# Kernel optimization log

Hardware: AMD Instinct MI355X
Metric: run time of the kernel (lower is better)

The kernel has to match this reference:

```python
import jax, jax.numpy as jnp
import numpy as np

B, T, E, H = 8, 2048, 1024, 64

def setup_inputs() -> dict:
    key = jax.random.key(0)
    k1, k2, k3, k4 = jax.random.split(key, 4)
    x = jax.random.normal(k1, (B, T, E), dtype=jnp.float32)
    # Linear(E, H, bias=False) weights stored as [E, H] (x @ W)
    s = 1.0 / np.sqrt(E)
    Wk = jax.random.normal(k2, (E, H), dtype=jnp.float32) * s
    Wq = jax.random.normal(k3, (E, H), dtype=jnp.float32) * s
    Wv = jax.random.normal(k4, (E, H), dtype=jnp.float32) * s
    return {"x": x, "Wk": Wk, "Wq": Wq, "Wv": Wv}

def reference(x, Wk, Wq, Wv):
    _, t, e = x.shape
    k = jnp.einsum('bte,eh->bth', x, Wk)
    q = jnp.einsum('bte,eh->bth', x, Wq)
    v = jnp.einsum('bte,eh->bth', x, Wv)
    # NOTE: original scales by E**-0.5 (embedding dim), not head_size**-0.5
    wei = jnp.einsum('bqh,bkh->bqk', q, k) * (e ** -0.5)
    causal = jnp.tril(jnp.ones((t, t), dtype=bool))
    wei = jnp.where(causal, wei, -jnp.inf)
    wei = jax.nn.softmax(wei, axis=-1)
    out = jnp.einsum('bqk,bkh->bqh', wei, v)
    return out
```

## Files before the change

kernel.cpp:

```cpp
#include <hip/hip_runtime.h>

typedef unsigned short u16;
typedef unsigned int u32;
typedef __bf16 bf16x8 __attribute__((ext_vector_type(8)));
typedef __bf16 bf16x4 __attribute__((ext_vector_type(4)));
typedef float f32x4 __attribute__((ext_vector_type(4)));

constexpr int Bn = 8, Tn = 2048, En = 1024, Hn = 64;
constexpr int Mrows = Bn * Tn;
constexpr float CEXP = 0.03125f * 1.4426950408889634f;

__device__ __forceinline__ u16 f2bf(float f) {
  u32 u = __float_as_uint(f);
  return (u16)((u + 0x7fffu + ((u >> 16) & 1u)) >> 16);
}

__device__ __forceinline__ void gload16(const void* g, void* l) {
  __builtin_amdgcn_global_load_lds(
      (const __attribute__((address_space(1))) void*)g,
      (__attribute__((address_space(3))) void*)l, 16, 0, 0);
}

__global__ __launch_bounds__(256) void wt_kernel(
    const float* __restrict__ Wk, const float* __restrict__ Wq,
    const float* __restrict__ Wv, u16* __restrict__ Wt) {
  __shared__ u16 tile[64][72];
  const int mat = blockIdx.x >> 4;
  const int k0 = (blockIdx.x & 15) * 64;
  const float* W = (mat == 0) ? Wk : (mat == 1) ? Wq : Wv;
  const int t = threadIdx.x;
  {
    const int kl = t >> 2;
    const int h0 = (t & 3) * 16;
    const float4* src = (const float4*)(W + (size_t)(k0 + kl) * Hn + h0);
#pragma unroll
    for (int i = 0; i < 4; ++i) {
      float4 v = src[i];
      tile[h0 + 4 * i + 0][kl] = f2bf(v.x);
      tile[h0 + 4 * i + 1][kl] = f2bf(v.y);
      tile[h0 + 4 * i + 2][kl] = f2bf(v.z);
      tile[h0 + 4 * i + 3][kl] = f2bf(v.w);
    }
  }
  __syncthreads();
  {
    const int hl = t >> 2;
    const int kk = (t & 3) * 16;
    uint4 a = *(const uint4*)&tile[hl][kk];
    uint4 b = *(const uint4*)&tile[hl][kk + 8];
    u16* dst = Wt + (size_t)mat * Hn * En + (size_t)hl * En + k0 + kk;
    *(uint4*)dst = a;
    *(uint4*)(dst + 8) = b;
  }
}

__global__ __launch_bounds__(256, 2) void qkv_kernel(
    const float* __restrict__ x, const u16* __restrict__ Wt,
    u16* __restrict__ Kb16, u16* __restrict__ Qb16, u16* __restrict__ Vt16) {
  constexpr int BK = 64;
  __shared__ __align__(16) float xs[3][32 * BK];
  const int t = threadIdx.x;
  const int w = t >> 6, lane = t & 63;
  const int quad = lane >> 4, l16 = lane & 15;
  const int r0 = blockIdx.x * 32;

  const int rj0 = w * 8 + (lane >> 4);
  const int rj1 = rj0 + 4;
  const float* gsrc0 = x + (size_t)(r0 + rj0) * En + (((lane & 15) ^ (rj0 & 15)) << 2);
  const float* gsrc1 = x + (size_t)(r0 + rj1) * En + (((lane & 15) ^ (rj1 & 15)) << 2);

  const u16* wpb = Wt + (size_t)l16 * En + quad * 8;

  int ofs[2][2];
#pragma unroll
  for (int ks = 0; ks < 2; ++ks) {
    ofs[ks][0] = ((ks * 8 + quad * 2) ^ l16) << 2;
    ofs[ks][1] = ((ks * 8 + quad * 2 + 1) ^ l16) << 2;
  }

  f32x4 acc[3][2];
#pragma unroll
  for (int i = 0; i < 3; ++i)
#pragma unroll
    for (int nt = 0; nt < 2; ++nt) acc[i][nt] = (f32x4){0.f, 0.f, 0.f, 0.f};

  bf16x8 afA[3][2], afB[3][2];

#define STAGE(P, K0)                              \
  do {                                            \
    gload16(gsrc0 + (K0), (P) + w * 512);         \
    gload16(gsrc1 + (K0), (P) + w * 512 + 256);   \
  } while (0)

#define LOADA(DST, K0)                                                              \
  do {                                                                              \
    _Pragma("unroll") for (int i_ = 0; i_ < 3; ++i_)                                \
        _Pragma("unroll") for (int ks_ = 0; ks_ < 2; ++ks_)                         \
            DST[i_][ks_] = *(const bf16x8*)(wpb + (size_t)((3 * w + i_) * 16) * En + \
                                            (K0) + ks_ * 32);                       \
  } while (0)

#define CVT8(LO, HI, R)                                       \
  do {                                                        \
    R[0] = (__bf16)LO[0]; R[1] = (__bf16)LO[1];               \
    R[2] = (__bf16)LO[2]; R[3] = (__bf16)LO[3];               \
    R[4] = (__bf16)HI[0]; R[5] = (__bf16)HI[1];               \
    R[6] = (__bf16)HI[2]; R[7] = (__bf16)HI[3];               \
  } while (0)

#define COMPUTE(P, AF)                                                             \
  do {                                                                             \
    const float* xa_ = (P) + l16 * 64;                                             \
    const float* xb_ = (P) + (l16 + 16) * 64;                                      \
    _Pragma("unroll") for (int ks_ = 0; ks_ < 2; ++ks_) {                          \
      f32x4 lo0_ = *(const f32x4*)(xa_ + ofs[ks_][0]);                             \
      f32x4 hi0_ = *(const f32x4*)(xa_ + ofs[ks_][1]);                             \
      f32x4 lo1_ = *(const f32x4*)(xb_ + ofs[ks_][0]);                             \
      f32x4 hi1_ = *(const f32x4*)(xb_ + ofs[ks_][1]);                             \
      bf16x8 b0_, b1_;                                                             \
      CVT8(lo0_, hi0_, b0_);                                                       \
      CVT8(lo1_, hi1_, b1_);                                                       \
      _Pragma("unroll") for (int i_ = 0; i_ < 3; ++i_) {                           \
        acc[i_][0] = __builtin_amdgcn_mfma_f32_16x16x32_bf16(AF[i_][ks_], b0_,     \
                                                             acc[i_][0], 0, 0, 0); \
        acc[i_][1] = __builtin_amdgcn_mfma_f32_16x16x32_bf16(AF[i_][ks_], b1_,     \
                                                             acc[i_][1], 0, 0, 0); \
      }                                                                            \
    }                                                                              \
  } while (0)

#define WAITBAR(N)                                          \
  do {                                                      \
    asm volatile("s_waitcnt vmcnt(" #N ")" ::: "memory");   \
    __builtin_amdgcn_s_barrier();                           \
    asm volatile("" ::: "memory");                          \
  } while (0)

  float* p0 = &xs[0][0];
  float* p1 = &xs[1][0];
  float* p2 = &xs[2][0];

  STAGE(p0, 0);
  STAGE(p1, BK);
  LOADA(afA, 0);

  for (int tt = 0; tt < 16; tt += 2) {
    WAITBAR(8);
    LOADA(afB, (tt + 1) * 64);
    asm volatile("" ::: "memory");
    if (tt + 2 < 16) STAGE(p2, (tt + 2) * 64);
    COMPUTE(p0, afA);

    if (tt == 14) {
      WAITBAR(6);
    } else {
      WAITBAR(8);
    }
    if (tt + 2 < 16) LOADA(afA, (tt + 2) * 64);
    asm volatile("" ::: "memory");
    if (tt + 3 < 16) STAGE(p0, (tt + 3) * 64);
    COMPUTE(p1, afB);

    float* tmp = p0; p0 = p2; p2 = p1; p1 = tmp;
  }

#undef STAGE
#undef LOADA
#undef CVT8
#undef COMPUTE
#undef WAITBAR

#pragma unroll
  for (int i = 0; i < 3; ++i) {
    const int mt = 3 * w + i;
    const int mat = mt >> 2, ht = mt & 3;
#pragma unroll
    for (int nt = 0; nt < 2; ++nt) {
      const int row = r0 + nt * 16 + l16;
      f32x4 a = acc[i][nt];
      if (mat < 2) {
        u16* dst = ((mat == 0) ? Kb16 : Qb16) + (size_t)row * Hn + ht * 16 + quad * 4;
        uint2 pk;
        pk.x = (u32)f2bf(a[0]) | ((u32)f2bf(a[1]) << 16);
        pk.y = (u32)f2bf(a[2]) | ((u32)f2bf(a[3]) << 16);
        *(uint2*)dst = pk;
      } else {
        const int bb = row >> 11, tt = row & 2047;
        u16* base = Vt16 + ((size_t)bb * 64) * Tn + tt;
#pragma unroll
        for (int r = 0; r < 4; ++r)
          base[(size_t)(ht * 16 + quad * 4 + r) * Tn] = f2bf(a[r]);
      }
    }
  }
}

__global__ __launch_bounds__(256, 4) void attn_kernel(
    const u16* __restrict__ Qb16, const u16* __restrict__ Kb16,
    const u16* __restrict__ Vt16, float* __restrict__ out) {
  __shared__ u16 pt[2][4][16][40];
  __shared__ float l_sh[4][16];
  __shared__ float o_sh[4][16][68];

  const int idx = blockIdx.x;
  const int b = idx & 7;
  const int tq = 127 - (idx >> 3);
  const int w = threadIdx.x >> 6, lane = threadIdx.x & 63;
  const int quad = lane >> 4, l16 = lane & 15;
  const int qbase = tq * 16;
  const int limit = qbase + 16;
  const int ch = ((limit + 127) >> 7) << 5;
  const int lo = w * ch;
  const int hi = min(lo + ch, limit);
  const int q_abs = qbase + l16;

  const u16* Kp = Kb16 + (size_t)b * Tn * Hn;
  const u16* Vp = Vt16 + (size_t)b * 64 * Tn;

  const u16* qrow = Qb16 + ((size_t)b * Tn + q_abs) * Hn + quad * 8;
  const bf16x8 qb0 = *(const bf16x8*)(qrow);
  const bf16x8 qb1 = *(const bf16x8*)(qrow + 32);

  f32x4 od0 = {0.f, 0.f, 0.f, 0.f}, od1 = od0, od2 = od0, od3 = od0;
  f32x4 lacc = {0.f, 0.f, 0.f, 0.f};

#pragma unroll 2
  for (int kb = lo; kb < hi; kb += 32) {
    const int par = (kb >> 5) & 1;
    const u16* krow0 = Kp + (size_t)(kb + l16) * Hn + quad * 8;
    const u16* krow1 = krow0 + (size_t)16 * Hn;
    f32x4 z = {0.f, 0.f, 0.f, 0.f};
    f32x4 st0 = __builtin_amdgcn_mfma_f32_16x16x32_bf16(*(const bf16x8*)(krow0), qb0, z, 0, 0, 0);
    st0 = __builtin_amdgcn_mfma_f32_16x16x32_bf16(*(const bf16x8*)(krow0 + 32), qb1, st0, 0, 0, 0);
    f32x4 st1 = __builtin_amdgcn_mfma_f32_16x16x32_bf16(*(const bf16x8*)(krow1), qb0, z, 0, 0, 0);
    st1 = __builtin_amdgcn_mfma_f32_16x16x32_bf16(*(const bf16x8*)(krow1 + 32), qb1, st1, 0, 0, 0);

    if (kb + 15 > qbase) {
#pragma unroll
      for (int r = 0; r < 4; ++r)
        if (kb + quad * 4 + r > q_abs) st0[r] = -3.0e38f;
    }
    if (kb + 31 > qbase) {
#pragma unroll
      for (int r = 0; r < 4; ++r)
        if (kb + 16 + quad * 4 + r > q_abs) st1[r] = -3.0e38f;
    }

    f32x4 p0, p1;
#pragma unroll
    for (int r = 0; r < 4; ++r) {
      p0[r] = __builtin_amdgcn_exp2f(st0[r] * CEXP);
      p1[r] = __builtin_amdgcn_exp2f(st1[r] * CEXP);
    }
    lacc += p0;
    lacc += p1;

    {
      bf16x4 w0, w1;
      w0[0] = (__bf16)p0[0]; w0[1] = (__bf16)p0[1];
      w0[2] = (__bf16)p0[2]; w0[3] = (__bf16)p0[3];
      w1[0] = (__bf16)p1[0]; w1[1] = (__bf16)p1[1];
      w1[2] = (__bf16)p1[2]; w1[3] = (__bf16)p1[3];
      *(bf16x4*)&pt[par][w][l16][quad * 4] = w0;
      *(bf16x4*)&pt[par][w][l16][16 + quad * 4] = w1;
    }
    const bf16x8 pb = *(const bf16x8*)&pt[par][w][l16][quad * 8];

    const u16* vrow = Vp + (size_t)l16 * Tn + kb + quad * 8;
    od0 = __builtin_amdgcn_mfma_f32_16x16x32_bf16(*(const bf16x8*)(vrow), pb, od0, 0, 0, 0);
    od1 = __builtin_amdgcn_mfma_f32_16x16x32_bf16(*(const bf16x8*)(vrow + (size_t)16 * Tn), pb, od1, 0, 0, 0);
    od2 = __builtin_amdgcn_mfma_f32_16x16x32_bf16(*(const bf16x8*)(vrow + (size_t)32 * Tn), pb, od2, 0, 0, 0);
    od3 = __builtin_amdgcn_mfma_f32_16x16x32_bf16(*(const bf16x8*)(vrow + (size_t)48 * Tn), pb, od3, 0, 0, 0);
  }

  float l = (lacc[0] + lacc[1]) + (lacc[2] + lacc[3]);
  l += __shfl_xor(l, 16);
  l += __shfl_xor(l, 32);
  if (quad == 0) l_sh[w][l16] = l;
  *(f32x4*)&o_sh[w][l16][0 * 16 + quad * 4] = od0;
  *(f32x4*)&o_sh[w][l16][1 * 16 + quad * 4] = od1;
  *(f32x4*)&o_sh[w][l16][2 * 16 + quad * 4] = od2;
  *(f32x4*)&o_sh[w][l16][3 * 16 + quad * 4] = od3;
  __syncthreads();

  const int qq = threadIdx.x >> 4, dq = threadIdx.x & 15;
  float lg = 0.f;
  f32x4 acc = {0.f, 0.f, 0.f, 0.f};
#pragma unroll
  for (int ww = 0; ww < 4; ++ww) {
    lg += l_sh[ww][qq];
    acc += *(const f32x4*)&o_sh[ww][qq][dq * 4];
  }
  acc *= (1.f / lg);
  *(f32x4*)(out + ((size_t)b * Tn + qbase + qq) * Hn + dq * 4) = acc;
}

extern "C" void kernel_launch(void* const* d_in, const int* in_sizes, int n_in,
                              void* d_out, int out_size, void* d_ws, size_t ws_size,
                              hipStream_t stream) {
  const void* x = nullptr;
  const void* Ws[3] = {nullptr, nullptr, nullptr};
  int wj = 0;
  for (int i = 0; i < n_in; ++i) {
    if (in_sizes[i] == Bn * Tn * En) x = d_in[i];
    else if (wj < 3) Ws[wj++] = d_in[i];
  }
  const float* Wk = (const float*)Ws[0];
  const float* Wq = (const float*)Ws[1];
  const float* Wv = (const float*)Ws[2];

  u16* Kb16 = (u16*)d_ws;
  u16* Qb16 = Kb16 + (size_t)Mrows * Hn;
  u16* Vt16 = Qb16 + (size_t)Mrows * Hn;
  u16* Wt   = Vt16 + (size_t)Mrows * Hn;

  wt_kernel<<<48, 256, 0, stream>>>(Wk, Wq, Wv, Wt);
  qkv_kernel<<<Mrows / 32, 256, 0, stream>>>((const float*)x, Wt, Kb16, Qb16, Vt16);
  attn_kernel<<<Bn * (Tn / 16), 256, 0, stream>>>(Qb16, Kb16, Vt16, (float*)d_out);
}
```

Before: 155.2 us.

## Process two 16-row query tiles per attention block to reuse K/V loads

Each attention block now handles 32 query rows (two 16-row tiles) instead of 16, so every K and V fragment loaded from global memory feeds MFMAs for both tiles. This halves the grid size and roughly halves K/V global traffic per query. In exchange, register pressure rises (eight output accumulators) and occupancy drops (launch bounds lowered from 4 to 2 blocks per CU). The second tile also computes some fully masked keys at the diagonal.

```diff
diff --git a/kernel.cpp b/kernel.cpp
--- a/kernel.cpp
+++ b/kernel.cpp
@@ -195,104 +195,161 @@
   }
 }
 
-__global__ __launch_bounds__(256, 4) void attn_kernel(
+__global__ __launch_bounds__(256, 2) void attn_kernel(
     const u16* __restrict__ Qb16, const u16* __restrict__ Kb16,
     const u16* __restrict__ Vt16, float* __restrict__ out) {
-  __shared__ u16 pt[2][4][16][40];
-  __shared__ float l_sh[4][16];
-  __shared__ float o_sh[4][16][68];
+  __shared__ u16 pt[2][4][2][16][40];
+  __shared__ float l_sh[2][4][16];
+  __shared__ float o_sh[2][4][16][68];
 
   const int idx = blockIdx.x;
   const int b = idx & 7;
-  const int tq = 127 - (idx >> 3);
+  const int tq = 63 - (idx >> 3);
   const int w = threadIdx.x >> 6, lane = threadIdx.x & 63;
   const int quad = lane >> 4, l16 = lane & 15;
-  const int qbase = tq * 16;
-  const int limit = qbase + 16;
+  const int qbase = tq * 32;
+  const int limit = qbase + 32;
   const int ch = ((limit + 127) >> 7) << 5;
   const int lo = w * ch;
   const int hi = min(lo + ch, limit);
-  const int q_abs = qbase + l16;
+  const int qa_abs = qbase + l16;
+  const int qb_abs = qbase + 16 + l16;
 
   const u16* Kp = Kb16 + (size_t)b * Tn * Hn;
   const u16* Vp = Vt16 + (size_t)b * 64 * Tn;
 
-  const u16* qrow = Qb16 + ((size_t)b * Tn + q_abs) * Hn + quad * 8;
-  const bf16x8 qb0 = *(const bf16x8*)(qrow);
-  const bf16x8 qb1 = *(const bf16x8*)(qrow + 32);
-
-  f32x4 od0 = {0.f, 0.f, 0.f, 0.f}, od1 = od0, od2 = od0, od3 = od0;
-  f32x4 lacc = {0.f, 0.f, 0.f, 0.f};
+  const u16* qrowA = Qb16 + ((size_t)b * Tn + qa_abs) * Hn + quad * 8;
+  const u16* qrowB = qrowA + (size_t)16 * Hn;
+  const bf16x8 qa0 = *(const bf16x8*)(qrowA);
+  const bf16x8 qa1 = *(const bf16x8*)(qrowA + 32);
+  const bf16x8 qb0 = *(const bf16x8*)(qrowB);
+  const bf16x8 qb1 = *(const bf16x8*)(qrowB + 32);
+
+  f32x4 oA0 = {0.f, 0.f, 0.f, 0.f}, oA1 = oA0, oA2 = oA0, oA3 = oA0;
+  f32x4 oB0 = oA0, oB1 = oA0, oB2 = oA0, oB3 = oA0;
+  f32x4 laccA = oA0, laccB = oA0;
 
 #pragma unroll 2
   for (int kb = lo; kb < hi; kb += 32) {
     const int par = (kb >> 5) & 1;
     const u16* krow0 = Kp + (size_t)(kb + l16) * Hn + quad * 8;
     const u16* krow1 = krow0 + (size_t)16 * Hn;
-    f32x4 z = {0.f, 0.f, 0.f, 0.f};
-    f32x4 st0 = __builtin_amdgcn_mfma_f32_16x16x32_bf16(*(const bf16x8*)(krow0), qb0, z, 0, 0, 0);
-    st0 = __builtin_amdgcn_mfma_f32_16x16x32_bf16(*(const bf16x8*)(krow0 + 32), qb1, st0, 0, 0, 0);
-    f32x4 st1 = __builtin_amdgcn_mfma_f32_16x16x32_bf16(*(const bf16x8*)(krow1), qb0, z, 0, 0, 0);
-    st1 = __builtin_amdgcn_mfma_f32_16x16x32_bf16(*(const bf16x8*)(krow1 + 32), qb1, st1, 0, 0, 0);
+    const bf16x8 k0lo = *(const bf16x8*)(krow0);
+    const bf16x8 k0hi = *(const bf16x8*)(krow0 + 32);
+    const bf16x8 k1lo = *(const bf16x8*)(krow1);
+    const bf16x8 k1hi = *(const bf16x8*)(krow1 + 32);
+
+    const f32x4 z = {0.f, 0.f, 0.f, 0.f};
+    f32x4 s0a = __builtin_amdgcn_mfma_f32_16x16x32_bf16(k0lo, qa0, z, 0, 0, 0);
+    s0a = __builtin_amdgcn_mfma_f32_16x16x32_bf16(k0hi, qa1, s0a, 0, 0, 0);
+    f32x4 s1a = __builtin_amdgcn_mfma_f32_16x16x32_bf16(k1lo, qa0, z, 0, 0, 0);
+    s1a = __builtin_amdgcn_mfma_f32_16x16x32_bf16(k1hi, qa1, s1a, 0, 0, 0);
+    f32x4 s0b = __builtin_amdgcn_mfma_f32_16x16x32_bf16(k0lo, qb0, z, 0, 0, 0);
+    s0b = __builtin_amdgcn_mfma_f32_16x16x32_bf16(k0hi, qb1, s0b, 0, 0, 0);
+    f32x4 s1b = __builtin_amdgcn_mfma_f32_16x16x32_bf16(k1lo, qb0, z, 0, 0, 0);
+    s1b = __builtin_amdgcn_mfma_f32_16x16x32_bf16(k1hi, qb1, s1b, 0, 0, 0);
 
     if (kb + 15 > qbase) {
 #pragma unroll
       for (int r = 0; r < 4; ++r)
-        if (kb + quad * 4 + r > q_abs) st0[r] = -3.0e38f;
+        if (kb + quad * 4 + r > qa_abs) s0a[r] = -3.0e38f;
     }
     if (kb + 31 > qbase) {
 #pragma unroll
       for (int r = 0; r < 4; ++r)
-        if (kb + 16 + quad * 4 + r > q_abs) st1[r] = -3.0e38f;
-    }
-
-    f32x4 p0, p1;
+        if (kb + 16 + quad * 4 + r > qa_abs) s1a[r] = -3.0e38f;
+    }
+    if (kb + 15 > qbase + 16) {
+#pragma unroll
+      for (int r = 0; r < 4; ++r)
+        if (kb + quad * 4 + r > qb_abs) s0b[r] = -3.0e38f;
+    }
+    if (kb + 31 > qbase + 16) {
+#pragma unroll
+      for (int r = 0; r < 4; ++r)
+        if (kb + 16 + quad * 4 + r > qb_abs) s1b[r] = -3.0e38f;
+    }
+
+    f32x4 pa0, pa1, pb0v, pb1v;
 #pragma unroll
     for (int r = 0; r < 4; ++r) {
-      p0[r] = __builtin_amdgcn_exp2f(st0[r] * CEXP);
-      p1[r] = __builtin_amdgcn_exp2f(st1[r] * CEXP);
-    }
-    lacc += p0;
-    lacc += p1;
+      pa0[r] = __builtin_amdgcn_exp2f(s0a[r] * CEXP);
+      pa1[r] = __builtin_amdgcn_exp2f(s1a[r] * CEXP);
+      pb0v[r] = __builtin_amdgcn_exp2f(s0b[r] * CEXP);
+      pb1v[r] = __builtin_amdgcn_exp2f(s1b[r] * CEXP);
+    }
+    laccA += pa0;
+    laccA += pa1;
+    laccB += pb0v;
+    laccB += pb1v;
 
     {
-      bf16x4 w0, w1;
-      w0[0] = (__bf16)p0[0]; w0[1] = (__bf16)p0[1];
-      w0[2] = (__bf16)p0[2]; w0[3] = (__bf16)p0[3];
-      w1[0] = (__bf16)p1[0]; w1[1] = (__bf16)p1[1];
-      w1[2] = (__bf16)p1[2]; w1[3] = (__bf16)p1[3];
-      *(bf16x4*)&pt[par][w][l16][quad * 4] = w0;
-      *(bf16x4*)&pt[par][w][l16][16 + quad * 4] = w1;
-    }
-    const bf16x8 pb = *(const bf16x8*)&pt[par][w][l16][quad * 8];
+      bf16x4 wa0, wa1, wb0, wb1;
+      wa0[0] = (__bf16)pa0[0]; wa0[1] = (__bf16)pa0[1];
+      wa0[2] = (__bf16)pa0[2]; wa0[3] = (__bf16)pa0[3];
+      wa1[0] = (__bf16)pa1[0]; wa1[1] = (__bf16)pa1[1];
+      wa1[2] = (__bf16)pa1[2]; wa1[3] = (__bf16)pa1[3];
+      wb0[0] = (__bf16)pb0v[0]; wb0[1] = (__bf16)pb0v[1];
+      wb0[2] = (__bf16)pb0v[2]; wb0[3] = (__bf16)pb0v[3];
+      wb1[0] = (__bf16)pb1v[0]; wb1[1] = (__bf16)pb1v[1];
+      wb1[2] = (__bf16)pb1v[2]; wb1[3] = (__bf16)pb1v[3];
+      *(bf16x4*)&pt[par][w][0][l16][quad * 4] = wa0;
+      *(bf16x4*)&pt[par][w][0][l16][16 + quad * 4] = wa1;
+      *(bf16x4*)&pt[par][w][1][l16][quad * 4] = wb0;
+      *(bf16x4*)&pt[par][w][1][l16][16 + quad * 4] = wb1;
+    }
+    const bf16x8 pba = *(const bf16x8*)&pt[par][w][0][l16][quad * 8];
+    const bf16x8 pbb = *(const bf16x8*)&pt[par][w][1][l16][quad * 8];
 
     const u16* vrow = Vp + (size_t)l16 * Tn + kb + quad * 8;
-    od0 = __builtin_amdgcn_mfma_f32_16x16x32_bf16(*(const bf16x8*)(vrow), pb, od0, 0, 0, 0);
-    od1 = __builtin_amdgcn_mfma_f32_16x16x32_bf16(*(const bf16x8*)(vrow + (size_t)16 * Tn), pb, od1, 0, 0, 0);
-    od2 = __builtin_amdgcn_mfma_f32_16x16x32_bf16(*(const bf16x8*)(vrow + (size_t)32 * Tn), pb, od2, 0, 0, 0);
-    od3 = __builtin_amdgcn_mfma_f32_16x16x32_bf16(*(const bf16x8*)(vrow + (size_t)48 * Tn), pb, od3, 0, 0, 0);
-  }
-
-  float l = (lacc[0] + lacc[1]) + (lacc[2] + lacc[3]);
-  l += __shfl_xor(l, 16);
-  l += __shfl_xor(l, 32);
-  if (quad == 0) l_sh[w][l16] = l;
-  *(f32x4*)&o_sh[w][l16][0 * 16 + quad * 4] = od0;
-  *(f32x4*)&o_sh[w][l16][1 * 16 + quad * 4] = od1;
-  *(f32x4*)&o_sh[w][l16][2 * 16 + quad * 4] = od2;
-  *(f32x4*)&o_sh[w][l16][3 * 16 + quad * 4] = od3;
+    const bf16x8 v0 = *(const bf16x8*)(vrow);
+    const bf16x8 v1 = *(const bf16x8*)(vrow + (size_t)16 * Tn);
+    const bf16x8 v2 = *(const bf16x8*)(vrow + (size_t)32 * Tn);
+    const bf16x8 v3 = *(const bf16x8*)(vrow + (size_t)48 * Tn);
+
+    oA0 = __builtin_amdgcn_mfma_f32_16x16x32_bf16(v0, pba, oA0, 0, 0, 0);
+    oA1 = __builtin_amdgcn_mfma_f32_16x16x32_bf16(v1, pba, oA1, 0, 0, 0);
+    oA2 = __builtin_amdgcn_mfma_f32_16x16x32_bf16(v2, pba, oA2, 0, 0, 0);
+    oA3 = __builtin_amdgcn_mfma_f32_16x16x32_bf16(v3, pba, oA3, 0, 0, 0);
+    oB0 = __builtin_amdgcn_mfma_f32_16x16x32_bf16(v0, pbb, oB0, 0, 0, 0);
+    oB1 = __builtin_amdgcn_mfma_f32_16x16x32_bf16(v1, pbb, oB1, 0, 0, 0);
+    oB2 = __builtin_amdgcn_mfma_f32_16x16x32_bf16(v2, pbb, oB2, 0, 0, 0);
+    oB3 = __builtin_amdgcn_mfma_f32_16x16x32_bf16(v3, pbb, oB3, 0, 0, 0);
+  }
+
+  float la = (laccA[0] + laccA[1]) + (laccA[2] + laccA[3]);
+  la += __shfl_xor(la, 16);
+  la += __shfl_xor(la, 32);
+  float lb = (laccB[0] + laccB[1]) + (laccB[2] + laccB[3]);
+  lb += __shfl_xor(lb, 16);
+  lb += __shfl_xor(lb, 32);
+  if (quad == 0) {
+    l_sh[0][w][l16] = la;
+    l_sh[1][w][l16] = lb;
+  }
+  *(f32x4*)&o_sh[0][w][l16][0 * 16 + quad * 4] = oA0;
+  *(f32x4*)&o_sh[0][w][l16][1 * 16 + quad * 4] = oA1;
+  *(f32x4*)&o_sh[0][w][l16][2 * 16 + quad * 4] = oA2;
+  *(f32x4*)&o_sh[0][w][l16][3 * 16 + quad * 4] = oA3;
+  *(f32x4*)&o_sh[1][w][l16][0 * 16 + quad * 4] = oB0;
+  *(f32x4*)&o_sh[1][w][l16][1 * 16 + quad * 4] = oB1;
+  *(f32x4*)&o_sh[1][w][l16][2 * 16 + quad * 4] = oB2;
+  *(f32x4*)&o_sh[1][w][l16][3 * 16 + quad * 4] = oB3;
   __syncthreads();
 
   const int qq = threadIdx.x >> 4, dq = threadIdx.x & 15;
-  float lg = 0.f;
-  f32x4 acc = {0.f, 0.f, 0.f, 0.f};
-#pragma unroll
-  for (int ww = 0; ww < 4; ++ww) {
-    lg += l_sh[ww][qq];
-    acc += *(const f32x4*)&o_sh[ww][qq][dq * 4];
-  }
-  acc *= (1.f / lg);
-  *(f32x4*)(out + ((size_t)b * Tn + qbase + qq) * Hn + dq * 4) = acc;
+#pragma unroll
+  for (int tl = 0; tl < 2; ++tl) {
+    float lg = 0.f;
+    f32x4 acc = {0.f, 0.f, 0.f, 0.f};
+#pragma unroll
+    for (int ww = 0; ww < 4; ++ww) {
+      lg += l_sh[tl][ww][qq];
+      acc += *(const f32x4*)&o_sh[tl][ww][qq][dq * 4];
+    }
+    acc *= (1.f / lg);
+    *(f32x4*)(out + ((size_t)b * Tn + qbase + tl * 16 + qq) * Hn + dq * 4) = acc;
+  }
 }
 
 extern "C" void kernel_launch(void* const* d_in, const int* in_sizes, int n_in,
@@ -316,5 +373,5 @@
 
   wt_kernel<<<48, 256, 0, stream>>>(Wk, Wq, Wv, Wt);
   qkv_kernel<<<Mrows / 32, 256, 0, stream>>>((const float*)x, Wt, Kb16, Qb16, Vt16);
-  attn_kernel<<<Bn * (Tn / 16), 256, 0, stream>>>(Qb16, Kb16, Vt16, (float*)d_out);
-}
+  attn_kernel<<<Bn * (Tn / 32), 256, 0, stream>>>(Qb16, Kb16, Vt16, (float*)d_out);
+}
```

Result: faster. 142.8 us (-8.0%).
